# Optimization experiments

Measured on AMD Instinct MI355X. Metric: run time of the kernel, lower is better.

## Reference

```python
import jax, jax.numpy as jnp
import numpy as np

N_E = 8192
E_DIM = 256
BETA = 0.25


def setup_inputs() -> dict:
    key = jax.random.key(0)
    k1, k2 = jax.random.split(key)
    z = jax.random.normal(k1, (16, E_DIM, 32, 32), dtype=jnp.float32)
    # nn.Embedding init: uniform(-1/n_e, 1/n_e)
    e_w = jax.random.uniform(k2, (N_E, E_DIM), dtype=jnp.float32,
                             minval=-1.0 / N_E, maxval=1.0 / N_E)
    return {"z": z, "e_w": e_w}


def reference(z, e_w):
    B, C, H, W = z.shape  # C == e_dim
    n_e = e_w.shape[0]
    # (B,C,H,W) -> (N, D)
    z_flat = jnp.transpose(z, (0, 2, 3, 1)).reshape(-1, C)
    # squared euclidean distances: ||z||^2 + ||e||^2 - 2 z.e  -> (N, n_e)
    z_sq = jnp.sum(z_flat * z_flat, axis=1, keepdims=True)
    e_sq = jnp.sum(e_w * e_w, axis=1)
    distances = z_sq + e_sq[None, :] - 2.0 * (z_flat @ e_w.T)
    indices = jnp.argmin(distances, axis=1)  # (N,)
    one_hot = jax.nn.one_hot(indices, n_e, dtype=z.dtype)  # (N, n_e)
    # one_hot @ e_w == gather
    z_q_flat = e_w[indices]
    z_q = jnp.transpose(z_q_flat.reshape(B, H, W, C), (0, 3, 1, 2))
    sg = jax.lax.stop_gradient
    loss_embed = jnp.mean((sg(z_q) - z) ** 2)
    loss_commit = jnp.mean((z_q - sg(z)) ** 2)
    loss = loss_embed + BETA * loss_commit
    # straight-through estimator
    z_q_st = z + sg(z_q - z)
    avg_probs = jnp.mean(one_hot, axis=0)
    perplexity = jnp.exp(-jnp.sum(avg_probs * jnp.log(avg_probs + 1e-10)))
    return loss, z_q_st, perplexity, one_hot, indices
```

## Files before the change

### kernel.cpp

```cpp
#include <hip/hip_runtime.h>
#include <hip/hip_bf16.h>
#include <math.h>

#define N_ROWS 16384
#define DIM    256
#define NE     8192
#define QMARGIN 21

#define SOFF 4194308

typedef __bf16 bf16x8 __attribute__((ext_vector_type(8)));
typedef float  f32x4  __attribute__((ext_vector_type(4)));
typedef float  vf4    __attribute__((ext_vector_type(4)));

__device__ __forceinline__ void gload_lds16(const __bf16* g, __bf16* l) {
  __builtin_amdgcn_global_load_lds(
      (const __attribute__((address_space(1))) unsigned int*)g,
      (__attribute__((address_space(3))) unsigned int*)l, 16, 0, 0);
}

__global__ void k_prep(const float* __restrict__ z, float* __restrict__ zf,
                       __bf16* __restrict__ zfb) {
  __shared__ float tile[32][33];
  int ct = blockIdx.x, ht = blockIdx.y, b = blockIdx.z;
  int tx = threadIdx.x & 31, ty = threadIdx.x >> 5;
  int c0 = ct * 32, hw0 = ht * 32;
  const size_t zb = (size_t)b * 256 * 1024;
#pragma unroll
  for (int p = 0; p < 4; ++p) {
    int c = p * 8 + ty;
    tile[c][tx] = z[zb + (size_t)(c0 + c) * 1024 + hw0 + tx];
  }
  __syncthreads();
#pragma unroll
  for (int p = 0; p < 4; ++p) {
    int r = p * 8 + ty;
    zf[(size_t)(b * 1024 + hw0 + r) * DIM + c0 + tx] = tile[tx][r];
  }
  if (threadIdx.x < 128) {
    int r = threadIdx.x >> 2, kc = threadIdx.x & 3;
    int row = b * 1024 + hw0 + r;
    bf16x8 v;
#pragma unroll
    for (int j = 0; j < 8; ++j) v[j] = (__bf16)tile[kc * 8 + j][r];
    int tn = row >> 7, g = (row >> 4) & 7, m15 = row & 15, kt = c0 >> 5;
    *(bf16x8*)(zfb + (size_t)tn * 32768 + kt * 4096 + g * 512 + (kc * 16 + m15) * 8) = v;
  }
}

__global__ void k_cvt_e(const float* __restrict__ ew, __bf16* __restrict__ ewb) {
  int gid = blockIdx.x * 256 + threadIdx.x;
  int r = gid >> 5, kc8 = gid & 31;
  const float* s = ew + (size_t)r * DIM + kc8 * 8;
  float4 v0 = *(const float4*)s, v1 = *(const float4*)(s + 4);
  bf16x8 v = {(__bf16)v0.x, (__bf16)v0.y, (__bf16)v0.z, (__bf16)v0.w,
              (__bf16)v1.x, (__bf16)v1.y, (__bf16)v1.z, (__bf16)v1.w};
  int t = r >> 7, g = (r >> 4) & 7, m15 = r & 15, kt = kc8 >> 2, kc = kc8 & 3;
  *(bf16x8*)(ewb + (size_t)t * 32768 + kt * 4096 + g * 512 + (kc * 16 + m15) * 8) = v;
}

__global__ __launch_bounds__(256, 2) void k_score(const __bf16* __restrict__ zfb,
                                                  const __bf16* __restrict__ ewb,
                                                  int2* __restrict__ part2) {
  __shared__ __align__(16) __bf16 Afull[32768];
  __shared__ __align__(16) __bf16 Bs[2][4096];
  const int tid = threadIdx.x;
  const int lane = tid & 63, wave = tid >> 6;
  const int wm = wave >> 1, wn = wave & 1;
  const int quad = lane >> 4, l15 = lane & 15;
  const int bx = blockIdx.x, byc = blockIdx.y;
  const __bf16* Ag = zfb + (size_t)bx * 32768;
  const __bf16* Bg = ewb + (size_t)byc * 262144;

  {
    const int base = wave * 8192;
#pragma unroll
    for (int i = 0; i < 16; ++i)
      gload_lds16(Ag + base + i * 512 + lane * 8, Afull + base + i * 512);
  }
  {
    const int boff = wave * 1024;
    gload_lds16(Bg + boff + lane * 8, Bs[0] + boff);
    gload_lds16(Bg + boff + 512 + lane * 8, Bs[0] + boff + 512);
  }

  f32x4 acc[4][4];
#pragma unroll
  for (int i = 0; i < 4; ++i)
#pragma unroll
    for (int j = 0; j < 4; ++j) acc[i][j] = (f32x4){0.f, 0.f, 0.f, 0.f};
  int r1[16], r2[16];
#pragma unroll
  for (int i = 0; i < 16; ++i) { r1[i] = 0x7fffffff; r2[i] = 0x7fffffff; }

  for (int it = 0; it < 64; ++it) {
    const int bt = it >> 3, kt = it & 7, buf = it & 1;
    __syncthreads();
    if (it < 63) {
      const int nx = it + 1;
      const __bf16* src = Bg + (nx >> 3) * 32768 + (nx & 7) * 4096 + wave * 1024;
      gload_lds16(src + lane * 8, Bs[buf ^ 1] + wave * 1024);
      gload_lds16(src + 512 + lane * 8, Bs[buf ^ 1] + wave * 1024 + 512);
    }
    bf16x8 af[4], bfr[4];
#pragma unroll
    for (int mi = 0; mi < 4; ++mi)
      af[mi] = *(const bf16x8*)(Afull + kt * 4096 + (wm * 4 + mi) * 512 + lane * 8);
#pragma unroll
    for (int ni = 0; ni < 4; ++ni)
      bfr[ni] = *(const bf16x8*)(Bs[buf] + (wn * 4 + ni) * 512 + lane * 8);
#pragma unroll
    for (int mi = 0; mi < 4; ++mi)
#pragma unroll
      for (int ni = 0; ni < 4; ++ni)
        acc[mi][ni] = __builtin_amdgcn_mfma_f32_16x16x32_bf16(af[mi], bfr[ni],
                                                              acc[mi][ni], 0, 0, 0);
    if (kt == 7) {
      const int colb = byc * 1024 + bt * 128 + wn * 64;
#pragma unroll
      for (int mi = 0; mi < 4; ++mi) {
#pragma unroll
        for (int rg = 0; rg < 4; ++rg) {
          const int idx = mi * 4 + rg;
          float s0 = -2.f * acc[mi][0][rg], s1 = -2.f * acc[mi][1][rg];
          float s2 = -2.f * acc[mi][2][rg], s3 = -2.f * acc[mi][3][rg];
          int q0 = min(max((int)((s0 + 1.0f) * 131072.0f), 0), 262143);
          int q1 = min(max((int)((s1 + 1.0f) * 131072.0f), 0), 262143);
          int q2 = min(max((int)((s2 + 1.0f) * 131072.0f), 0), 262143);
          int q3 = min(max((int)((s3 + 1.0f) * 131072.0f), 0), 262143);
          int k0 = (q0 << 13) | (colb + l15);
          int k1 = (q1 << 13) | (colb + 16 + l15);
          int k2 = (q2 << 13) | (colb + 32 + l15);
          int k3 = (q3 << 13) | (colb + 48 + l15);
          int a = min(k0, k1), bb = max(k0, k1);
          int c = min(k2, k3), dd = max(k2, k3);
          int t1 = min(a, c);
          int t2 = min(max(a, c), min(bb, dd));
          int n1 = min(r1[idx], t1);
          int n2 = min(max(r1[idx], t1), min(r2[idx], t2));
          r1[idx] = n1; r2[idx] = n2;
        }
      }
#pragma unroll
      for (int i = 0; i < 4; ++i)
#pragma unroll
        for (int j = 0; j < 4; ++j) acc[i][j] = (f32x4){0.f, 0.f, 0.f, 0.f};
    }
  }

#pragma unroll
  for (int mi = 0; mi < 4; ++mi) {
#pragma unroll
    for (int rg = 0; rg < 4; ++rg) {
      const int idx = mi * 4 + rg;
      int k1 = r1[idx], k2 = r2[idx];
#pragma unroll
      for (int d = 1; d < 16; d <<= 1) {
        int o1 = __shfl_xor(k1, d), o2 = __shfl_xor(k2, d);
        k2 = min(max(k1, o1), min(k2, o2));
        k1 = min(k1, o1);
      }
      if (l15 == 0) {
        int row = bx * 128 + wm * 64 + mi * 16 + quad * 4 + rg;
        int2 v; v.x = k1; v.y = k2;
        part2[row * 16 + byc * 2 + wn] = v;
      }
    }
  }
}

__device__ __forceinline__ float np_sumsq_128(const float* __restrict__ p) {
  float r[8];
#pragma unroll
  for (int j = 0; j < 8; ++j) r[j] = __fmul_rn(p[j], p[j]);
  for (int i = 8; i < 128; i += 8) {
#pragma unroll
    for (int j = 0; j < 8; ++j) r[j] = __fadd_rn(r[j], __fmul_rn(p[i + j], p[i + j]));
  }
  return __fadd_rn(__fadd_rn(__fadd_rn(r[0], r[1]), __fadd_rn(r[2], r[3])),
                   __fadd_rn(__fadd_rn(r[4], r[5]), __fadd_rn(r[6], r[7])));
}

__global__ __launch_bounds__(256) void k_pick(const int2* __restrict__ part2,
                                              const float* __restrict__ zf,
                                              const float* __restrict__ ew,
                                              float* __restrict__ idxF,
                                              float* __restrict__ losspart) {
  __shared__ int cand[4][40];
  __shared__ int cnts[4];
  const int t = threadIdx.x, lane = t & 63, wv = t >> 6;
  const int row = blockIdx.x * 4 + wv;
  if (lane == 0) cnts[wv] = 0;
  int2 pv;
  if (lane < 16) pv = part2[row * 16 + lane];
  else { pv.x = 0x7fffffff; pv.y = 0x7fffffff; }
  int kmin = pv.x;
#pragma unroll
  for (int d = 1; d < 64; d <<= 1) kmin = min(kmin, __shfl_xor(kmin, d));
  const int qthr = min((kmin >> 13) + QMARGIN, 262143);
  const int kthr = (qthr << 13) | 8191;
  __syncthreads();
  if (lane < 16) {
    if (pv.x <= kthr) { int p = atomicAdd(&cnts[wv], 1); cand[wv][p] = pv.x & 8191; }
    if (pv.y <= kthr) { int p = atomicAdd(&cnts[wv], 1); cand[wv][p] = pv.y & 8191; }
  }
  __syncthreads();
  const int cnt = cnts[wv];
  const float* zr = zf + (size_t)row * DIM;
  float bd = INFINITY; int bj = 0x7fffffff;
  if (lane < cnt) {
    int j = cand[wv][lane];
    const float* e = ew + (size_t)j * DIM;
    float acc = 0.f;
    for (int k = 0; k < DIM; ++k) acc = __builtin_fmaf(zr[k], e[k], acc);
    float esq = __fadd_rn(np_sumsq_128(e), np_sumsq_128(e + 128));
    float zsq = __fadd_rn(np_sumsq_128(zr), np_sumsq_128(zr + 128));
    bd = __fsub_rn(__fadd_rn(zsq, esq), __fmul_rn(2.0f, acc));
    bj = j;
  }
#pragma unroll
  for (int d = 1; d < 64; d <<= 1) {
    float od = __shfl_xor(bd, d); int oj = __shfl_xor(bj, d);
    if (od < bd || (od == bd && oj < bj)) { bd = od; bj = oj; }
  }
  int c = lane * 4;
  float4 e4 = *reinterpret_cast<const float4*>(ew + (size_t)bj * DIM + c);
  float4 z4 = *reinterpret_cast<const float4*>(zr + c);
  float t0 = __fsub_rn(e4.x, z4.x), t1 = __fsub_rn(e4.y, z4.y);
  float t2 = __fsub_rn(e4.z, z4.z), t3 = __fsub_rn(e4.w, z4.w);
  float s = __fadd_rn(__fadd_rn(__fmul_rn(t0, t0), __fmul_rn(t1, t1)),
                      __fadd_rn(__fmul_rn(t2, t2), __fmul_rn(t3, t3)));
#pragma unroll
  for (int d = 1; d < 64; d <<= 1) s += __shfl_xor(s, d);
  if (lane == 0) {
    idxF[row] = (float)bj;
    losspart[row] = s;
  }
}

__global__ __launch_bounds__(256) void k_scalars(const float* __restrict__ idxF,
                                                 const float* __restrict__ losspart,
                                                 float* __restrict__ out) {
  __shared__ int hist[NE];
  __shared__ float red[256];
  int t = threadIdx.x;
  for (int i = t; i < NE; i += 256) hist[i] = 0;
  __syncthreads();
  float ls = 0.f;
  for (int i = t; i < N_ROWS; i += 256) {
    atomicAdd(&hist[(int)idxF[i]], 1);
    ls += losspart[i];
  }
  __syncthreads();
  float es = 0.f;
  for (int i = t; i < NE; i += 256) {
    float p = (float)hist[i] * (1.0f / 16384.0f);
    es += p * logf(p + 1e-10f);
  }
  red[t] = es; __syncthreads();
  for (int w = 128; w > 0; w >>= 1) { if (t < w) red[t] += red[t + w]; __syncthreads(); }
  float esum = red[0]; __syncthreads();
  red[t] = ls; __syncthreads();
  for (int w = 128; w > 0; w >>= 1) { if (t < w) red[t] += red[t + w]; __syncthreads(); }
  if (t == 0) {
    out[4194305] = expf(-esum);
    float m = red[0] * (1.0f / 4194304.0f);
    out[0] = __fadd_rn(m, __fmul_rn(0.25f, m));
  }
}

__global__ void k_zq_out(const float* __restrict__ z, const float* __restrict__ ew,
                         const float* __restrict__ idxF, float* __restrict__ out) {
  __shared__ float tileE[32][33];
  __shared__ int sidx[32];
  int ct = blockIdx.x, ht = blockIdx.y, b = blockIdx.z;
  int tx = threadIdx.x & 31, ty = threadIdx.x >> 5;
  int c0 = ct * 32, hw0 = ht * 32;
  if (threadIdx.x < 32) sidx[threadIdx.x] = (int)idxF[b * 1024 + hw0 + threadIdx.x];
  __syncthreads();
#pragma unroll
  for (int p = 0; p < 4; ++p) {
    int r = p * 8 + ty;
    tileE[tx][r] = ew[(size_t)sidx[r] * DIM + c0 + tx];
  }
  __syncthreads();
  float* outq = out + 1;
#pragma unroll
  for (int p = 0; p < 4; ++p) {
    int cl = p * 8 + ty;
    size_t gi = (size_t)(b * 256 + c0 + cl) * 1024 + hw0 + tx;
    float zv = z[gi];
    outq[gi] = __fadd_rn(zv, __fsub_rn(tileE[cl][tx], zv));
  }
}

__global__ void k_onehot(const float* __restrict__ idxF, float* __restrict__ out) {
  int row = blockIdx.x;
  int t = threadIdx.x;
  int idx = (int)idxF[row];
  float* p = out + 4194306 + (size_t)row * NE;
  if (t == 0) {
    float2 h; h.x = (0 == idx) ? 1.f : 0.f; h.y = (1 == idx) ? 1.f : 0.f;
    *(float2*)p = h;
    float2 q; q.x = (8190 == idx) ? 1.f : 0.f; q.y = (8191 == idx) ? 1.f : 0.f;
    *(float2*)(p + 8190) = q;
  }
  vf4* b4 = (vf4*)(p + 2);
#pragma unroll
  for (int it = 0; it < 8; ++it) {
    int i = it * 256 + t;
    if (i < 2047) {
      int c = 2 + i * 4;
      vf4 v;
      v.x = (c     == idx) ? 1.f : 0.f;
      v.y = (c + 1 == idx) ? 1.f : 0.f;
      v.z = (c + 2 == idx) ? 1.f : 0.f;
      v.w = (c + 3 == idx) ? 1.f : 0.f;
      __builtin_nontemporal_store(v, b4 + i);
    }
  }
}

extern "C" void kernel_launch(void* const* d_in, const int* in_sizes, int n_in,
                              void* d_out, int out_size, void* d_ws, size_t ws_size,
                              hipStream_t stream) {
  const float* z  = (const float*)d_in[0];
  const float* ew = (const float*)d_in[1];
  float* out = (float*)d_out;
  float*  zf    = out + SOFF;
  __bf16* zfb   = (__bf16*)(out + SOFF + 4194304);
  __bf16* ewb   = (__bf16*)(out + SOFF + 6291456);
  int2*   part2 = (int2*)(out + SOFF + 7340032);
  float*  lprt  = out + SOFF + 7864320;
  float*  idxF  = out + 138412034;

  k_prep<<<dim3(8, 32, 16), 256, 0, stream>>>(z, zf, zfb);
  k_cvt_e<<<dim3(1024), 256, 0, stream>>>(ew, ewb);
  k_score<<<dim3(128, 8), 256, 0, stream>>>(zfb, ewb, part2);
  k_pick<<<dim3(4096), 256, 0, stream>>>(part2, zf, ew, idxF, lprt);
  k_scalars<<<1, 256, 0, stream>>>(idxF, lprt, out);
  k_zq_out<<<dim3(8, 32, 16), 256, 0, stream>>>(z, ew, idxF, out);
  k_onehot<<<dim3(16384), 256, 0, stream>>>(idxF, out);
}
```

Baseline: 923.6 us.

## Stream codebook tiles into registers, drop LDS sync, build histogram in pick kernel

The score kernel now loads codebook fragments straight from global memory into registers, two steps ahead, instead of double-buffering them through LDS with a barrier every iteration. The k-loop is fully unrolled and the quantisation step becomes a single FMA without clamping. The histogram moves from the single-block scalars kernel into k_pick via global atomics, with the buffer cleared by a memset. This removes per-iteration barriers and the serial single-block histogram. In exchange, the two waves sharing a column half both fetch the same codebook data from global or cache, and with the clamp gone, out-of-range scores now rely on conversion saturation and could corrupt the packed keys.

```diff
diff --git a/kernel.cpp b/kernel.cpp
--- a/kernel.cpp
+++ b/kernel.cpp
@@ -63,14 +63,13 @@
                                                   const __bf16* __restrict__ ewb,
                                                   int2* __restrict__ part2) {
   __shared__ __align__(16) __bf16 Afull[32768];
-  __shared__ __align__(16) __bf16 Bs[2][4096];
   const int tid = threadIdx.x;
   const int lane = tid & 63, wave = tid >> 6;
   const int wm = wave >> 1, wn = wave & 1;
   const int quad = lane >> 4, l15 = lane & 15;
   const int bx = blockIdx.x, byc = blockIdx.y;
   const __bf16* Ag = zfb + (size_t)bx * 32768;
-  const __bf16* Bg = ewb + (size_t)byc * 262144;
+  const __bf16* Bg = ewb + (size_t)byc * 262144 + wn * 2048 + lane * 8;
 
   {
     const int base = wave * 8192;
@@ -78,11 +77,11 @@
     for (int i = 0; i < 16; ++i)
       gload_lds16(Ag + base + i * 512 + lane * 8, Afull + base + i * 512);
   }
-  {
-    const int boff = wave * 1024;
-    gload_lds16(Bg + boff + lane * 8, Bs[0] + boff);
-    gload_lds16(Bg + boff + 512 + lane * 8, Bs[0] + boff + 512);
-  }
+  bf16x8 pf[2][4];
+#pragma unroll
+  for (int ni = 0; ni < 4; ++ni) pf[0][ni] = *(const bf16x8*)(Bg + ni * 512);
+#pragma unroll
+  for (int ni = 0; ni < 4; ++ni) pf[1][ni] = *(const bf16x8*)(Bg + 4096 + ni * 512);
 
   f32x4 acc[4][4];
 #pragma unroll
@@ -93,59 +92,57 @@
 #pragma unroll
   for (int i = 0; i < 16; ++i) { r1[i] = 0x7fffffff; r2[i] = 0x7fffffff; }
 
-  for (int it = 0; it < 64; ++it) {
-    const int bt = it >> 3, kt = it & 7, buf = it & 1;
-    __syncthreads();
-    if (it < 63) {
-      const int nx = it + 1;
-      const __bf16* src = Bg + (nx >> 3) * 32768 + (nx & 7) * 4096 + wave * 1024;
-      gload_lds16(src + lane * 8, Bs[buf ^ 1] + wave * 1024);
-      gload_lds16(src + 512 + lane * 8, Bs[buf ^ 1] + wave * 1024 + 512);
+  __syncthreads();
+
+  for (int bt = 0; bt < 8; ++bt) {
+#pragma unroll
+    for (int kt = 0; kt < 8; ++kt) {
+      const int it = bt * 8 + kt;
+      const int b = it & 1;
+      bf16x8 af[4];
+#pragma unroll
+      for (int mi = 0; mi < 4; ++mi)
+        af[mi] = *(const bf16x8*)(Afull + kt * 4096 + (wm * 4 + mi) * 512 + lane * 8);
+#pragma unroll
+      for (int mi = 0; mi < 4; ++mi)
+#pragma unroll
+        for (int ni = 0; ni < 4; ++ni)
+          acc[mi][ni] = __builtin_amdgcn_mfma_f32_16x16x32_bf16(af[mi], pf[b][ni],
+                                                                acc[mi][ni], 0, 0, 0);
+      if (it < 62) {
+        const int nx = it + 2;
+        const __bf16* src = Bg + (nx >> 3) * 32768 + (nx & 7) * 4096;
+#pragma unroll
+        for (int ni = 0; ni < 4; ++ni) pf[b][ni] = *(const bf16x8*)(src + ni * 512);
+      }
     }
-    bf16x8 af[4], bfr[4];
-#pragma unroll
-    for (int mi = 0; mi < 4; ++mi)
-      af[mi] = *(const bf16x8*)(Afull + kt * 4096 + (wm * 4 + mi) * 512 + lane * 8);
-#pragma unroll
-    for (int ni = 0; ni < 4; ++ni)
-      bfr[ni] = *(const bf16x8*)(Bs[buf] + (wn * 4 + ni) * 512 + lane * 8);
-#pragma unroll
-    for (int mi = 0; mi < 4; ++mi)
-#pragma unroll
-      for (int ni = 0; ni < 4; ++ni)
-        acc[mi][ni] = __builtin_amdgcn_mfma_f32_16x16x32_bf16(af[mi], bfr[ni],
-                                                              acc[mi][ni], 0, 0, 0);
-    if (kt == 7) {
-      const int colb = byc * 1024 + bt * 128 + wn * 64;
-#pragma unroll
-      for (int mi = 0; mi < 4; ++mi) {
-#pragma unroll
-        for (int rg = 0; rg < 4; ++rg) {
-          const int idx = mi * 4 + rg;
-          float s0 = -2.f * acc[mi][0][rg], s1 = -2.f * acc[mi][1][rg];
-          float s2 = -2.f * acc[mi][2][rg], s3 = -2.f * acc[mi][3][rg];
-          int q0 = min(max((int)((s0 + 1.0f) * 131072.0f), 0), 262143);
-          int q1 = min(max((int)((s1 + 1.0f) * 131072.0f), 0), 262143);
-          int q2 = min(max((int)((s2 + 1.0f) * 131072.0f), 0), 262143);
-          int q3 = min(max((int)((s3 + 1.0f) * 131072.0f), 0), 262143);
-          int k0 = (q0 << 13) | (colb + l15);
-          int k1 = (q1 << 13) | (colb + 16 + l15);
-          int k2 = (q2 << 13) | (colb + 32 + l15);
-          int k3 = (q3 << 13) | (colb + 48 + l15);
-          int a = min(k0, k1), bb = max(k0, k1);
-          int c = min(k2, k3), dd = max(k2, k3);
-          int t1 = min(a, c);
-          int t2 = min(max(a, c), min(bb, dd));
-          int n1 = min(r1[idx], t1);
-          int n2 = min(max(r1[idx], t1), min(r2[idx], t2));
-          r1[idx] = n1; r2[idx] = n2;
-        }
+    const int colb = byc * 1024 + bt * 128 + wn * 64;
+#pragma unroll
+    for (int mi = 0; mi < 4; ++mi) {
+#pragma unroll
+      for (int rg = 0; rg < 4; ++rg) {
+        const int idx = mi * 4 + rg;
+        int q0 = (int)__builtin_fmaf(acc[mi][0][rg], -262144.f, 131072.f);
+        int q1 = (int)__builtin_fmaf(acc[mi][1][rg], -262144.f, 131072.f);
+        int q2 = (int)__builtin_fmaf(acc[mi][2][rg], -262144.f, 131072.f);
+        int q3 = (int)__builtin_fmaf(acc[mi][3][rg], -262144.f, 131072.f);
+        int k0 = (q0 << 13) | (colb + l15);
+        int k1 = (q1 << 13) | (colb + 16 + l15);
+        int k2 = (q2 << 13) | (colb + 32 + l15);
+        int k3 = (q3 << 13) | (colb + 48 + l15);
+        int a = min(k0, k1), bb = max(k0, k1);
+        int c = min(k2, k3), dd = max(k2, k3);
+        int t1 = min(a, c);
+        int t2 = min(max(a, c), min(bb, dd));
+        int n1 = min(r1[idx], t1);
+        int n2 = min(max(r1[idx], t1), min(r2[idx], t2));
+        r1[idx] = n1; r2[idx] = n2;
       }
-#pragma unroll
-      for (int i = 0; i < 4; ++i)
-#pragma unroll
-        for (int j = 0; j < 4; ++j) acc[i][j] = (f32x4){0.f, 0.f, 0.f, 0.f};
     }
+#pragma unroll
+    for (int i = 0; i < 4; ++i)
+#pragma unroll
+      for (int j = 0; j < 4; ++j) acc[i][j] = (f32x4){0.f, 0.f, 0.f, 0.f};
   }
 
 #pragma unroll
@@ -185,7 +182,8 @@
                                               const float* __restrict__ zf,
                                               const float* __restrict__ ew,
                                               float* __restrict__ idxF,
-                                              float* __restrict__ losspart) {
+                                              float* __restrict__ losspart,
+                                              int* __restrict__ ghist) {
   __shared__ int cand[4][40];
   __shared__ int cnts[4];
   const int t = threadIdx.x, lane = t & 63, wv = t >> 6;
@@ -235,28 +233,22 @@
   if (lane == 0) {
     idxF[row] = (float)bj;
     losspart[row] = s;
-  }
-}
-
-__global__ __launch_bounds__(256) void k_scalars(const float* __restrict__ idxF,
+    atomicAdd(&ghist[bj], 1);
+  }
+}
+
+__global__ __launch_bounds__(256) void k_scalars(const int* __restrict__ ghist,
                                                  const float* __restrict__ losspart,
                                                  float* __restrict__ out) {
-  __shared__ int hist[NE];
   __shared__ float red[256];
   int t = threadIdx.x;
-  for (int i = t; i < NE; i += 256) hist[i] = 0;
-  __syncthreads();
-  float ls = 0.f;
-  for (int i = t; i < N_ROWS; i += 256) {
-    atomicAdd(&hist[(int)idxF[i]], 1);
-    ls += losspart[i];
-  }
-  __syncthreads();
   float es = 0.f;
   for (int i = t; i < NE; i += 256) {
-    float p = (float)hist[i] * (1.0f / 16384.0f);
+    float p = (float)ghist[i] * (1.0f / 16384.0f);
     es += p * logf(p + 1e-10f);
   }
+  float ls = 0.f;
+  for (int i = t; i < N_ROWS; i += 256) ls += losspart[i];
   red[t] = es; __syncthreads();
   for (int w = 128; w > 0; w >>= 1) { if (t < w) red[t] += red[t + w]; __syncthreads(); }
   float esum = red[0]; __syncthreads();
@@ -332,13 +324,15 @@
   __bf16* ewb   = (__bf16*)(out + SOFF + 6291456);
   int2*   part2 = (int2*)(out + SOFF + 7340032);
   float*  lprt  = out + SOFF + 7864320;
+  int*    ghist = (int*)(out + SOFF + 7880704);
   float*  idxF  = out + 138412034;
 
+  hipMemsetAsync(ghist, 0, NE * sizeof(int), stream);
   k_prep<<<dim3(8, 32, 16), 256, 0, stream>>>(z, zf, zfb);
   k_cvt_e<<<dim3(1024), 256, 0, stream>>>(ew, ewb);
   k_score<<<dim3(128, 8), 256, 0, stream>>>(zfb, ewb, part2);
-  k_pick<<<dim3(4096), 256, 0, stream>>>(part2, zf, ew, idxF, lprt);
-  k_scalars<<<1, 256, 0, stream>>>(idxF, lprt, out);
+  k_pick<<<dim3(4096), 256, 0, stream>>>(part2, zf, ew, idxF, lprt, ghist);
+  k_scalars<<<1, 256, 0, stream>>>(ghist, lprt, out);
   k_zq_out<<<dim3(8, 32, 16), 256, 0, stream>>>(z, ew, idxF, out);
   k_onehot<<<dim3(16384), 256, 0, stream>>>(idxF, out);
 }
```

Measured after the change: 938.2 us. Within noise of the previous version (+1.6%).
